# Performance work log

Hardware: AMD Instinct MI355X
Metric: run time of the kernel (lower is better)

## Reference

```python
import jax, jax.numpy as jnp
import numpy as np


def setup_inputs() -> dict:
    key = jax.random.key(0)
    ks = jax.random.split(key, 7)
    B, S, E = 2, 4096, 512
    return {
        "query": jax.random.normal(ks[0], (B, S, E), jnp.float32),
        "key": jax.random.normal(ks[1], (B, S, E), jnp.float32),
        "value": jax.random.normal(ks[2], (B, S, E), jnp.float32),
        "in_proj_weight": jax.random.normal(ks[3], (3 * E, E), jnp.float32) * 0.02,
        "in_proj_bias": jax.random.normal(ks[4], (3 * E,), jnp.float32) * 0.02,
        "out_proj_weight": jax.random.normal(ks[5], (E, E), jnp.float32) * 0.02,
        "out_proj_bias": jax.random.normal(ks[6], (E,), jnp.float32) * 0.02,
        "window_size": 512,
        "stride": 256,
    }


def reference(query, key, value, in_proj_weight, in_proj_bias,
              out_proj_weight, out_proj_bias, window_size, stride):
    B, S, E = query.shape
    H = 8
    hd = E // H
    scale = 1.0 / np.sqrt(hd).astype(np.float32)

    # Project full sequences once (equivalent to projecting each window slice).
    wq, wk, wv = in_proj_weight[:E], in_proj_weight[E:2 * E], in_proj_weight[2 * E:]
    bq, bk, bv = in_proj_bias[:E], in_proj_bias[E:2 * E], in_proj_bias[2 * E:]
    qp = query @ wq.T + bq   # [B,S,E]
    kp = key @ wk.T + bk
    vp = value @ wv.T + bv

    # Overlapping window gather: [nw, W] token indices.
    starts = np.arange(0, S - window_size + 1, stride)
    idx = starts[:, None] + np.arange(window_size)[None, :]  # [nw, W]
    nw, W = idx.shape

    def heads(x):  # [B,S,E] -> [B,nw,W,H,hd]
        return x[:, idx].reshape(B, nw, W, H, hd)

    qh, kh, vh = heads(qp), heads(kp), heads(vp)

    scores = jnp.einsum('bnqhd,bnkhd->bnhqk', qh, kh) * scale  # [B,nw,H,W,W]
    probs = jax.nn.softmax(scores, axis=-1)
    ctx = jnp.einsum('bnhqk,bnkhd->bnqhd', probs, vh)           # [B,nw,W,H,hd]
    ctx = ctx.reshape(B, nw * W, E)                             # concat over windows
    return ctx @ out_proj_weight.T + out_proj_bias              # [B, nw*W, E]
```

## Files before the change

kernel.cpp:

```cpp
#include <hip/hip_runtime.h>
#include <hip/hip_bf16.h>

typedef __bf16 bf16x8 __attribute__((ext_vector_type(8)));
typedef float f32x4 __attribute__((ext_vector_type(4)));
typedef float f32x16 __attribute__((ext_vector_type(16)));

__device__ __forceinline__ ushort f2bf(float f) {
  union { float f; unsigned u; } x; x.f = f;
  unsigned r = x.u + 0x7fffu + ((x.u >> 16) & 1u);
  return (ushort)(r >> 16);
}

__device__ __forceinline__ void gld_lds16(const void* g, void* l) {
  __builtin_amdgcn_global_load_lds(
      (const __attribute__((address_space(1))) void*)g,
      (__attribute__((address_space(3))) void*)l, 16, 0, 0);
}

__global__ __launch_bounds__(256) void k_cvt_w(
    const float* __restrict__ wi, const float* __restrict__ wo,
    ushort* __restrict__ dst) {
  const int NWI = 196608, NWO = 65536;
  const int total = NWI + NWO;
  int i = blockIdx.x * 256 + threadIdx.x;
  int stride = gridDim.x * 256;
  for (; i < total; i += stride) {
    const float* s; int j;
    if (i < NWI) { s = wi; j = i; }
    else         { s = wo; j = i - NWI; }
    float4 val = reinterpret_cast<const float4*>(s)[j];
    ushort4 o;
    o.x = f2bf(val.x); o.y = f2bf(val.y); o.z = f2bf(val.z); o.w = f2bf(val.w);
    reinterpret_cast<ushort4*>(dst)[i] = o;
  }
}

#define GK 512
#define GN 512

__global__ __launch_bounds__(256) void k_gemm_qkv(
    const float* __restrict__ za0, const float* __restrict__ za1,
    const float* __restrict__ za2,
    const ushort* __restrict__ Btbase,
    const float* __restrict__ biasbase,
    ushort* __restrict__ Cbase, float qs)
{
  int z = blockIdx.z;
  const float* A32 = (z == 0) ? za0 : (z == 1) ? za1 : za2;
  const ushort* Bt = Btbase + (size_t)262144 * z;
  const float* bias = biasbase + 512 * z;
  float osc = (z == 0) ? qs : 1.0f;

  __shared__ float  As[128 * 32];
  __shared__ ushort Bs[128 * 32];

  int tid = threadIdx.x;
  int wv = tid >> 6, ln = tid & 63;
  int l15 = ln & 15, lg = ln >> 4;
  int wm = wv >> 1, wn = wv & 1;
  int m0 = blockIdx.x * 128, n0 = blockIdx.y * 128;

  f32x4 acc[4][4] = {};

  for (int kt = 0; kt < 16; ++kt) {
    __syncthreads();
#pragma unroll
    for (int it = 0; it < 4; ++it) {
      int s = it * 256 + tid;
      int row = s >> 3;
      int cs = (s & 7) * 16;
      int gofs = (cs ^ ((row & 7) << 4)) >> 2;
      gld_lds16(A32 + (size_t)(m0 + row) * GK + kt * 32 + gofs,
                (char*)As + (it * 256 + wv * 64) * 16);
    }
#pragma unroll
    for (int h2 = 0; h2 < 2; ++h2) {
      int c = h2 * 256 + wv * 64 + ln;
      int row = c >> 2, kc = (c & 3) * 8;
      gld_lds16(Bt + (size_t)(n0 + row) * GK + kt * 32 + kc,
                (char*)Bs + (h2 * 256 + wv * 64) * 16);
    }
    __syncthreads();

    bf16x8 af[4], bf4[4];
#pragma unroll
    for (int mf = 0; mf < 4; ++mf) {
      int row = wm * 64 + mf * 16 + l15;
      int xr = (row & 7) << 4;
      const char* rb = (const char*)As + row * 128;
      float4 x0 = *reinterpret_cast<const float4*>(rb + ((lg * 32) ^ xr));
      float4 x1 = *reinterpret_cast<const float4*>(rb + (((lg * 32) + 16) ^ xr));
      uint w0, w1, w2, w3;
      asm("v_cvt_pk_bf16_f32 %0, %1, %2" : "=v"(w0) : "v"(x0.x), "v"(x0.y));
      asm("v_cvt_pk_bf16_f32 %0, %1, %2" : "=v"(w1) : "v"(x0.z), "v"(x0.w));
      asm("v_cvt_pk_bf16_f32 %0, %1, %2" : "=v"(w2) : "v"(x1.x), "v"(x1.y));
      asm("v_cvt_pk_bf16_f32 %0, %1, %2" : "=v"(w3) : "v"(x1.z), "v"(x1.w));
      union { uint u[4]; bf16x8 v; } t;
      t.u[0] = w0; t.u[1] = w1; t.u[2] = w2; t.u[3] = w3;
      af[mf] = t.v;
    }
#pragma unroll
    for (int nf = 0; nf < 4; ++nf)
      bf4[nf] = *reinterpret_cast<const bf16x8*>(&Bs[(wn * 64 + nf * 16 + l15) * 32 + lg * 8]);
#pragma unroll
    for (int mf = 0; mf < 4; ++mf)
#pragma unroll
      for (int nf = 0; nf < 4; ++nf)
        acc[mf][nf] = __builtin_amdgcn_mfma_f32_16x16x32_bf16(af[mf], bf4[nf], acc[mf][nf], 0, 0, 0);
  }

#pragma unroll
  for (int mf = 0; mf < 4; ++mf)
#pragma unroll
    for (int nf = 0; nf < 4; ++nf)
#pragma unroll
      for (int r = 0; r < 4; ++r) {
        int rr = m0 + wm * 64 + mf * 16 + lg * 4 + r;
        int cc = n0 + wn * 64 + nf * 16 + l15;
        float v = (acc[mf][nf][r] + bias[cc]) * osc;
        (Cbase + (size_t)4194304 * z)[(size_t)rr * GN + cc] = f2bf(v);
      }
}

__global__ __launch_bounds__(256) void k_gemm_out(
    const ushort* __restrict__ Ab, const ushort* __restrict__ Bt,
    const float* __restrict__ bias, float* __restrict__ C)
{
  __shared__ ushort As[128 * 32];
  __shared__ ushort Bs[128 * 32];

  int tid = threadIdx.x;
  int wv = tid >> 6, ln = tid & 63;
  int l15 = ln & 15, lg = ln >> 4;
  int wm = wv >> 1, wn = wv & 1;
  int m0 = blockIdx.x * 128, n0 = blockIdx.y * 128;

  f32x4 acc[4][4] = {};

  for (int kt = 0; kt < GK / 32; ++kt) {
    __syncthreads();
#pragma unroll
    for (int h2 = 0; h2 < 2; ++h2) {
      int c = h2 * 256 + wv * 64 + ln;
      int row = c >> 2, kc = (c & 3) * 8;
      gld_lds16(Ab + (size_t)(m0 + row) * GK + kt * 32 + kc,
                (char*)As + (h2 * 256 + wv * 64) * 16);
      gld_lds16(Bt + (size_t)(n0 + row) * GK + kt * 32 + kc,
                (char*)Bs + (h2 * 256 + wv * 64) * 16);
    }
    __syncthreads();
    bf16x8 af[4], bf4[4];
#pragma unroll
    for (int mf = 0; mf < 4; ++mf)
      af[mf] = *reinterpret_cast<const bf16x8*>(&As[(wm * 64 + mf * 16 + l15) * 32 + lg * 8]);
#pragma unroll
    for (int nf = 0; nf < 4; ++nf)
      bf4[nf] = *reinterpret_cast<const bf16x8*>(&Bs[(wn * 64 + nf * 16 + l15) * 32 + lg * 8]);
#pragma unroll
    for (int mf = 0; mf < 4; ++mf)
#pragma unroll
      for (int nf = 0; nf < 4; ++nf)
        acc[mf][nf] = __builtin_amdgcn_mfma_f32_16x16x32_bf16(af[mf], bf4[nf], acc[mf][nf], 0, 0, 0);
  }

#pragma unroll
  for (int mf = 0; mf < 4; ++mf)
#pragma unroll
    for (int nf = 0; nf < 4; ++nf)
#pragma unroll
      for (int r = 0; r < 4; ++r) {
        int rr = m0 + wm * 64 + mf * 16 + lg * 4 + r;
        int cc = n0 + wn * 64 + nf * 16 + l15;
        C[(size_t)rr * GN + cc] = acc[mf][nf][r] + bias[cc];
      }
}

__global__ __launch_bounds__(256, 2) void k_attn(
    const ushort* __restrict__ qp, const ushort* __restrict__ kp,
    const ushort* __restrict__ vp, ushort* __restrict__ ctx)
{
  const int E = 512, SEQ = 4096;
  int bid0 = blockIdx.x;
  int bid = (bid0 & 7) * 60 + (bid0 >> 3);
  int qh = bid & 1;
  int h = (bid >> 1) & 7;
  int n = (bid >> 4) % 15;
  int b = bid / 240;
  int start = n * 256;

  int tid = threadIdx.x;
  int w = tid >> 6, ln = tid & 63;
  int l31 = ln & 31, hi = ln >> 5;

  size_t base = ((size_t)(b * SEQ + start)) * E + h * 64;
  const ushort* Kw = kp + base;
  const ushort* Vw = vp + base;
  const ushort* Qw = qp + base;

  __shared__ ushort Vt[32768];

  {
    int sk = (tid & 63) * 8;
    int sd = (tid >> 6) * 16;
    const ushort* src = Vw + (size_t)sk * E + sd;
    union { uint4 q[2]; ushort u[16]; } R0, R1, R2, R3, R4, R5, R6, R7;
    R0.q[0] = *(const uint4*)(src + 0 * E); R0.q[1] = *(const uint4*)(src + 0 * E + 8);
    R1.q[0] = *(const uint4*)(src + 1 * E); R1.q[1] = *(const uint4*)(src + 1 * E + 8);
    R2.q[0] = *(const uint4*)(src + 2 * E); R2.q[1] = *(const uint4*)(src + 2 * E + 8);
    R3.q[0] = *(const uint4*)(src + 3 * E); R3.q[1] = *(const uint4*)(src + 3 * E + 8);
    R4.q[0] = *(const uint4*)(src + 4 * E); R4.q[1] = *(const uint4*)(src + 4 * E + 8);
    R5.q[0] = *(const uint4*)(src + 5 * E); R5.q[1] = *(const uint4*)(src + 5 * E + 8);
    R6.q[0] = *(const uint4*)(src + 6 * E); R6.q[1] = *(const uint4*)(src + 6 * E + 8);
    R7.q[0] = *(const uint4*)(src + 7 * E); R7.q[1] = *(const uint4*)(src + 7 * E + 8);
#pragma unroll
    for (int d0 = 0; d0 < 16; ++d0) {
      int d = sd + d0;
      uint4 val;
      val.x = (uint)R0.u[d0] | ((uint)R1.u[d0] << 16);
      val.y = (uint)R2.u[d0] | ((uint)R3.u[d0] << 16);
      val.z = (uint)R4.u[d0] | ((uint)R5.u[d0] << 16);
      val.w = (uint)R6.u[d0] | ((uint)R7.u[d0] << 16);
      int off = d * 1024 + ((sk * 2) ^ ((d & 7) << 4));
      *(uint4*)((char*)Vt + off) = val;
    }
  }
  __syncthreads();

  int q0 = qh * 256 + w * 64;

  bf16x8 qa0, qa1, qa2, qa3, qb0, qb1, qb2, qb3;
  {
    const ushort* qra = Qw + (size_t)(q0 + l31) * E + hi * 8;
    const ushort* qrb = qra + (size_t)32 * E;
    qa0 = *reinterpret_cast<const bf16x8*>(qra + 0);
    qa1 = *reinterpret_cast<const bf16x8*>(qra + 16);
    qa2 = *reinterpret_cast<const bf16x8*>(qra + 32);
    qa3 = *reinterpret_cast<const bf16x8*>(qra + 48);
    qb0 = *reinterpret_cast<const bf16x8*>(qrb + 0);
    qb1 = *reinterpret_cast<const bf16x8*>(qrb + 16);
    qb2 = *reinterpret_cast<const bf16x8*>(qrb + 32);
    qb3 = *reinterpret_cast<const bf16x8*>(qrb + 48);
  }

  f32x16 ca0 = {}, ca1 = {}, cb0_ = {}, cb1_ = {};
  float psa = 0.f, psb = 0.f;
  const char* lb = (const char*)Vt;

#pragma unroll
  for (int kb = 0; kb < 16; ++kb) {
    bf16x8 kf0, kf1, kf2, kf3;
    {
      const ushort* kr = Kw + (size_t)(kb * 32 + l31) * E + hi * 8;
      kf0 = *reinterpret_cast<const bf16x8*>(kr + 0);
      kf1 = *reinterpret_cast<const bf16x8*>(kr + 16);
      kf2 = *reinterpret_cast<const bf16x8*>(kr + 32);
      kf3 = *reinterpret_cast<const bf16x8*>(kr + 48);
    }
    bf16x8 vb00, vb01, vb10, vb11;
    {
      int row = l31, rowh = 32 + l31;
      int cb0 = kb * 64 + hi * 16;
      int cb1 = cb0 + 32;
      int xr0 = (row & 7) << 4;
      vb00 = *reinterpret_cast<const bf16x8*>(lb + row * 1024 + (cb0 ^ xr0));
      vb01 = *reinterpret_cast<const bf16x8*>(lb + rowh * 1024 + (cb0 ^ xr0));
      vb10 = *reinterpret_cast<const bf16x8*>(lb + row * 1024 + (cb1 ^ xr0));
      vb11 = *reinterpret_cast<const bf16x8*>(lb + rowh * 1024 + (cb1 ^ xr0));
    }

    f32x16 s1 = {}, s2 = {};
    __builtin_amdgcn_s_setprio(1);
    s1 = __builtin_amdgcn_mfma_f32_32x32x16_bf16(kf0, qa0, s1, 0, 0, 0);
    s2 = __builtin_amdgcn_mfma_f32_32x32x16_bf16(kf0, qb0, s2, 0, 0, 0);
    s1 = __builtin_amdgcn_mfma_f32_32x32x16_bf16(kf1, qa1, s1, 0, 0, 0);
    s2 = __builtin_amdgcn_mfma_f32_32x32x16_bf16(kf1, qb1, s2, 0, 0, 0);
    s1 = __builtin_amdgcn_mfma_f32_32x32x16_bf16(kf2, qa2, s1, 0, 0, 0);
    s2 = __builtin_amdgcn_mfma_f32_32x32x16_bf16(kf2, qb2, s2, 0, 0, 0);
    s1 = __builtin_amdgcn_mfma_f32_32x32x16_bf16(kf3, qa3, s1, 0, 0, 0);
    s2 = __builtin_amdgcn_mfma_f32_32x32x16_bf16(kf3, qb3, s2, 0, 0, 0);
    __builtin_amdgcn_s_setprio(0);

#pragma unroll
    for (int r = 0; r < 16; ++r) s1[r] = __builtin_amdgcn_exp2f(s1[r]);
#pragma unroll
    for (int r = 0; r < 16; ++r) s2[r] = __builtin_amdgcn_exp2f(s2[r]);
    {
      float t0 = (s1[0] + s1[1]) + (s1[2] + s1[3]);
      float t1 = (s1[4] + s1[5]) + (s1[6] + s1[7]);
      float t2 = (s1[8] + s1[9]) + (s1[10] + s1[11]);
      float t3 = (s1[12] + s1[13]) + (s1[14] + s1[15]);
      psa += (t0 + t1) + (t2 + t3);
      float u0 = (s2[0] + s2[1]) + (s2[2] + s2[3]);
      float u1 = (s2[4] + s2[5]) + (s2[6] + s2[7]);
      float u2 = (s2[8] + s2[9]) + (s2[10] + s2[11]);
      float u3 = (s2[12] + s2[13]) + (s2[14] + s2[15]);
      psb += (u0 + u1) + (u2 + u3);
    }

    uint a0, a1, a2, a3, a4, a5, a6, a7;
    asm("v_cvt_pk_bf16_f32 %0, %1, %2" : "=v"(a0) : "v"(s1[0]),  "v"(s1[1]));
    asm("v_cvt_pk_bf16_f32 %0, %1, %2" : "=v"(a1) : "v"(s1[2]),  "v"(s1[3]));
    asm("v_cvt_pk_bf16_f32 %0, %1, %2" : "=v"(a2) : "v"(s1[4]),  "v"(s1[5]));
    asm("v_cvt_pk_bf16_f32 %0, %1, %2" : "=v"(a3) : "v"(s1[6]),  "v"(s1[7]));
    asm("v_cvt_pk_bf16_f32 %0, %1, %2" : "=v"(a4) : "v"(s1[8]),  "v"(s1[9]));
    asm("v_cvt_pk_bf16_f32 %0, %1, %2" : "=v"(a5) : "v"(s1[10]), "v"(s1[11]));
    asm("v_cvt_pk_bf16_f32 %0, %1, %2" : "=v"(a6) : "v"(s1[12]), "v"(s1[13]));
    asm("v_cvt_pk_bf16_f32 %0, %1, %2" : "=v"(a7) : "v"(s1[14]), "v"(s1[15]));
    asm("v_permlane32_swap_b32 %0, %1" : "+v"(a0), "+v"(a2));
    asm("v_permlane32_swap_b32 %0, %1" : "+v"(a1), "+v"(a3));
    asm("v_permlane32_swap_b32 %0, %1" : "+v"(a4), "+v"(a6));
    asm("v_permlane32_swap_b32 %0, %1" : "+v"(a5), "+v"(a7));
    uint b0, b1, b2, b3, b4, b5, b6, b7;
    asm("v_cvt_pk_bf16_f32 %0, %1, %2" : "=v"(b0) : "v"(s2[0]),  "v"(s2[1]));
    asm("v_cvt_pk_bf16_f32 %0, %1, %2" : "=v"(b1) : "v"(s2[2]),  "v"(s2[3]));
    asm("v_cvt_pk_bf16_f32 %0, %1, %2" : "=v"(b2) : "v"(s2[4]),  "v"(s2[5]));
    asm("v_cvt_pk_bf16_f32 %0, %1, %2" : "=v"(b3) : "v"(s2[6]),  "v"(s2[7]));
    asm("v_cvt_pk_bf16_f32 %0, %1, %2" : "=v"(b4) : "v"(s2[8]),  "v"(s2[9]));
    asm("v_cvt_pk_bf16_f32 %0, %1, %2" : "=v"(b5) : "v"(s2[10]), "v"(s2[11]));
    asm("v_cvt_pk_bf16_f32 %0, %1, %2" : "=v"(b6) : "v"(s2[12]), "v"(s2[13]));
    asm("v_cvt_pk_bf16_f32 %0, %1, %2" : "=v"(b7) : "v"(s2[14]), "v"(s2[15]));
    asm("v_permlane32_swap_b32 %0, %1" : "+v"(b0), "+v"(b2));
    asm("v_permlane32_swap_b32 %0, %1" : "+v"(b1), "+v"(b3));
    asm("v_permlane32_swap_b32 %0, %1" : "+v"(b4), "+v"(b6));
    asm("v_permlane32_swap_b32 %0, %1" : "+v"(b5), "+v"(b7));
    union { uint u[4]; bf16x8 v; } A1, A2, B1, B2;
    A1.u[0] = a0; A1.u[1] = a1; A1.u[2] = a2; A1.u[3] = a3;
    A2.u[0] = a4; A2.u[1] = a5; A2.u[2] = a6; A2.u[3] = a7;
    B1.u[0] = b0; B1.u[1] = b1; B1.u[2] = b2; B1.u[3] = b3;
    B2.u[0] = b4; B2.u[1] = b5; B2.u[2] = b6; B2.u[3] = b7;

    __builtin_amdgcn_s_setprio(1);
    ca0  = __builtin_amdgcn_mfma_f32_32x32x16_bf16(A1.v, vb00, ca0, 0, 0, 0);
    cb0_ = __builtin_amdgcn_mfma_f32_32x32x16_bf16(B1.v, vb00, cb0_, 0, 0, 0);
    ca1  = __builtin_amdgcn_mfma_f32_32x32x16_bf16(A1.v, vb01, ca1, 0, 0, 0);
    cb1_ = __builtin_amdgcn_mfma_f32_32x32x16_bf16(B1.v, vb01, cb1_, 0, 0, 0);
    ca0  = __builtin_amdgcn_mfma_f32_32x32x16_bf16(A2.v, vb10, ca0, 0, 0, 0);
    cb0_ = __builtin_amdgcn_mfma_f32_32x32x16_bf16(B2.v, vb10, cb0_, 0, 0, 0);
    ca1  = __builtin_amdgcn_mfma_f32_32x32x16_bf16(A2.v, vb11, ca1, 0, 0, 0);
    cb1_ = __builtin_amdgcn_mfma_f32_32x32x16_bf16(B2.v, vb11, cb1_, 0, 0, 0);
    __builtin_amdgcn_s_setprio(0);
  }

  psa += __shfl_xor(psa, 32);
  psb += __shfl_xor(psb, 32);
  float ria = 1.0f / psa;
  float rib = 1.0f / psb;
  size_t orow0 = (size_t)b * 7680 + (size_t)n * 512 + q0;
#pragma unroll
  for (int r = 0; r < 16; ++r) {
    int qrel = (r & 3) + 8 * (r >> 2) + 4 * hi;
    float r1 = __shfl(ria, qrel);
    float r2 = __shfl(rib, qrel);
    ushort* dA = ctx + (orow0 + qrel) * E + h * 64 + l31;
    ushort* dB = ctx + (orow0 + 32 + qrel) * E + h * 64 + l31;
    dA[0]  = f2bf(ca0[r] * r1);
    dA[32] = f2bf(ca1[r] * r1);
    dB[0]  = f2bf(cb0_[r] * r2);
    dB[32] = f2bf(cb1_[r] * r2);
  }
}

extern "C" void kernel_launch(void* const* d_in, const int* in_sizes, int n_in,
                              void* d_out, int out_size, void* d_ws, size_t ws_size,
                              hipStream_t stream) {
  const float* query = (const float*)d_in[0];
  const float* key   = (const float*)d_in[1];
  const float* value = (const float*)d_in[2];
  const float* ipw   = (const float*)d_in[3];
  const float* ipb   = (const float*)d_in[4];
  const float* opw   = (const float*)d_in[5];
  const float* opb   = (const float*)d_in[6];

  ushort* wib = (ushort*)d_ws;
  ushort* wob = wib + 786432;
  ushort* qp  = wob + 262144;
  ushort* kp  = qp  + 4194304;
  ushort* vp  = kp  + 4194304;
  ushort* ctx = vp  + 4194304;

  const float SC = 0.125f * 1.44269504088896340736f;

  k_cvt_w<<<512, 256, 0, stream>>>(ipw, opw, wib);

  k_gemm_qkv<<<dim3(64, 4, 3), 256, 0, stream>>>(
      query, key, value, wib, ipb, qp, SC);

  k_attn<<<480, 256, 0, stream>>>(qp, kp, vp, ctx);

  k_gemm_out<<<dim3(120, 4, 1), 256, 0, stream>>>(
      ctx, wob, opb, (float*)d_out);
}
```

Before: 84.24 us.

## Software-pipeline QKV and output GEMMs with multi-buffered LDS and XCD-aware block swizzle

Result: faster. 81.72 us (-3.0%).

```diff
diff --git a/kernel.cpp b/kernel.cpp
--- a/kernel.cpp
+++ b/kernel.cpp
@@ -16,6 +16,13 @@
       (const __attribute__((address_space(1))) void*)g,
       (__attribute__((address_space(3))) void*)l, 16, 0, 0);
 }
+
+#define VMWAIT2 asm volatile("s_waitcnt vmcnt(2)" ::: "memory")
+#define VMWAIT4 asm volatile("s_waitcnt vmcnt(4)" ::: "memory")
+#define VMWAIT0 asm volatile("s_waitcnt vmcnt(0)" ::: "memory")
+#define LGKM0   asm volatile("s_waitcnt lgkmcnt(0)" ::: "memory")
+#define SCHEDB  __builtin_amdgcn_sched_barrier(0)
+#define RBAR    __builtin_amdgcn_s_barrier()
 
 __global__ __launch_bounds__(256) void k_cvt_w(
     const float* __restrict__ wi, const float* __restrict__ wo,
@@ -35,9 +42,6 @@
   }
 }
 
-#define GK 512
-#define GN 512
-
 __global__ __launch_bounds__(256) void k_gemm_qkv(
     const float* __restrict__ za0, const float* __restrict__ za1,
     const float* __restrict__ za2,
@@ -45,68 +49,106 @@
     const float* __restrict__ biasbase,
     ushort* __restrict__ Cbase, float qs)
 {
-  int z = blockIdx.z;
+  int bid0 = blockIdx.x;
+  int bid = (bid0 & 7) * 96 + (bid0 >> 3);
+  int yy = bid & 3;
+  int rest = bid >> 2;
+  int xx = rest & 63;
+  int z = rest >> 6;
+
   const float* A32 = (z == 0) ? za0 : (z == 1) ? za1 : za2;
   const ushort* Bt = Btbase + (size_t)262144 * z;
   const float* bias = biasbase + 512 * z;
   float osc = (z == 0) ? qs : 1.0f;
 
-  __shared__ float  As[128 * 32];
-  __shared__ ushort Bs[128 * 32];
+  __shared__ ushort As[2][4096];
+  __shared__ ushort Bs[3][4096];
 
   int tid = threadIdx.x;
   int wv = tid >> 6, ln = tid & 63;
   int l15 = ln & 15, lg = ln >> 4;
   int wm = wv >> 1, wn = wv & 1;
-  int m0 = blockIdx.x * 128, n0 = blockIdx.y * 128;
+  int m0 = xx * 128, n0 = yy * 128;
+
+  int row_s = tid >> 1, kh = (tid & 1) * 16;
+  const float* aP = A32 + (size_t)(m0 + row_s) * 512 + kh;
+  int ldsOff = row_s * 32 + kh;
+
+#define STAGE_B(KT, BUF)                                                      \
+  {                                                                           \
+    _Pragma("unroll")                                                         \
+    for (int h2 = 0; h2 < 2; ++h2) {                                          \
+      int c = h2 * 256 + wv * 64 + ln;                                        \
+      int row = c >> 2, kc = (c & 3) * 8;                                     \
+      gld_lds16(Bt + (size_t)(n0 + row) * 512 + (KT) * 32 + kc,               \
+                (char*)&Bs[BUF][0] + (h2 * 256 + wv * 64) * 16);              \
+    }                                                                         \
+  }
+
+#define CVT_WRITE_A(F0, F1, F2, F3, BUF)                                      \
+  {                                                                           \
+    uint w0, w1, w2, w3, w4, w5, w6, w7;                                      \
+    asm("v_cvt_pk_bf16_f32 %0, %1, %2" : "=v"(w0) : "v"(F0.x), "v"(F0.y));    \
+    asm("v_cvt_pk_bf16_f32 %0, %1, %2" : "=v"(w1) : "v"(F0.z), "v"(F0.w));    \
+    asm("v_cvt_pk_bf16_f32 %0, %1, %2" : "=v"(w2) : "v"(F1.x), "v"(F1.y));    \
+    asm("v_cvt_pk_bf16_f32 %0, %1, %2" : "=v"(w3) : "v"(F1.z), "v"(F1.w));    \
+    asm("v_cvt_pk_bf16_f32 %0, %1, %2" : "=v"(w4) : "v"(F2.x), "v"(F2.y));    \
+    asm("v_cvt_pk_bf16_f32 %0, %1, %2" : "=v"(w5) : "v"(F2.z), "v"(F2.w));    \
+    asm("v_cvt_pk_bf16_f32 %0, %1, %2" : "=v"(w6) : "v"(F3.x), "v"(F3.y));    \
+    asm("v_cvt_pk_bf16_f32 %0, %1, %2" : "=v"(w7) : "v"(F3.z), "v"(F3.w));    \
+    uint4 p0; p0.x = w0; p0.y = w1; p0.z = w2; p0.w = w3;                     \
+    uint4 p1; p1.x = w4; p1.y = w5; p1.z = w6; p1.w = w7;                     \
+    reinterpret_cast<uint4*>(&As[BUF][ldsOff])[0] = p0;                       \
+    reinterpret_cast<uint4*>(&As[BUF][ldsOff + 8])[0] = p1;                   \
+  }
 
   f32x4 acc[4][4] = {};
 
+  STAGE_B(0, 0);
+  float4 g0 = reinterpret_cast<const float4*>(aP)[0];
+  float4 g1 = reinterpret_cast<const float4*>(aP)[1];
+  float4 g2 = reinterpret_cast<const float4*>(aP)[2];
+  float4 g3 = reinterpret_cast<const float4*>(aP)[3];
+  STAGE_B(1, 1);
+  VMWAIT2; SCHEDB;
+  CVT_WRITE_A(g0, g1, g2, g3, 0);
+  LGKM0; SCHEDB;
+  RBAR;
+
+#pragma unroll
   for (int kt = 0; kt < 16; ++kt) {
-    __syncthreads();
-#pragma unroll
-    for (int it = 0; it < 4; ++it) {
-      int s = it * 256 + tid;
-      int row = s >> 3;
-      int cs = (s & 7) * 16;
-      int gofs = (cs ^ ((row & 7) << 4)) >> 2;
-      gld_lds16(A32 + (size_t)(m0 + row) * GK + kt * 32 + gofs,
-                (char*)As + (it * 256 + wv * 64) * 16);
-    }
-#pragma unroll
-    for (int h2 = 0; h2 < 2; ++h2) {
-      int c = h2 * 256 + wv * 64 + ln;
-      int row = c >> 2, kc = (c & 3) * 8;
-      gld_lds16(Bt + (size_t)(n0 + row) * GK + kt * 32 + kc,
-                (char*)Bs + (h2 * 256 + wv * 64) * 16);
-    }
-    __syncthreads();
+    const int cur = kt & 1;
+    const int bcur = kt % 3;
+    float4 f0, f1, f2, f3;
+    if (kt < 15) {
+      const float* ap = aP + (kt + 1) * 32;
+      f0 = reinterpret_cast<const float4*>(ap)[0];
+      f1 = reinterpret_cast<const float4*>(ap)[1];
+      f2 = reinterpret_cast<const float4*>(ap)[2];
+      f3 = reinterpret_cast<const float4*>(ap)[3];
+    }
+    if (kt < 14) STAGE_B(kt + 2, (kt + 2) % 3);
 
     bf16x8 af[4], bf4[4];
 #pragma unroll
-    for (int mf = 0; mf < 4; ++mf) {
-      int row = wm * 64 + mf * 16 + l15;
-      int xr = (row & 7) << 4;
-      const char* rb = (const char*)As + row * 128;
-      float4 x0 = *reinterpret_cast<const float4*>(rb + ((lg * 32) ^ xr));
-      float4 x1 = *reinterpret_cast<const float4*>(rb + (((lg * 32) + 16) ^ xr));
-      uint w0, w1, w2, w3;
-      asm("v_cvt_pk_bf16_f32 %0, %1, %2" : "=v"(w0) : "v"(x0.x), "v"(x0.y));
-      asm("v_cvt_pk_bf16_f32 %0, %1, %2" : "=v"(w1) : "v"(x0.z), "v"(x0.w));
-      asm("v_cvt_pk_bf16_f32 %0, %1, %2" : "=v"(w2) : "v"(x1.x), "v"(x1.y));
-      asm("v_cvt_pk_bf16_f32 %0, %1, %2" : "=v"(w3) : "v"(x1.z), "v"(x1.w));
-      union { uint u[4]; bf16x8 v; } t;
-      t.u[0] = w0; t.u[1] = w1; t.u[2] = w2; t.u[3] = w3;
-      af[mf] = t.v;
-    }
+    for (int mf = 0; mf < 4; ++mf)
+      af[mf] = *reinterpret_cast<const bf16x8*>(&As[cur][(wm * 64 + mf * 16 + l15) * 32 + lg * 8]);
 #pragma unroll
     for (int nf = 0; nf < 4; ++nf)
-      bf4[nf] = *reinterpret_cast<const bf16x8*>(&Bs[(wn * 64 + nf * 16 + l15) * 32 + lg * 8]);
+      bf4[nf] = *reinterpret_cast<const bf16x8*>(&Bs[bcur][(wn * 64 + nf * 16 + l15) * 32 + lg * 8]);
 #pragma unroll
     for (int mf = 0; mf < 4; ++mf)
 #pragma unroll
       for (int nf = 0; nf < 4; ++nf)
         acc[mf][nf] = __builtin_amdgcn_mfma_f32_16x16x32_bf16(af[mf], bf4[nf], acc[mf][nf], 0, 0, 0);
+
+    if (kt < 15) {
+      if (kt < 14) { VMWAIT2; } else { VMWAIT0; }
+      SCHEDB;
+      CVT_WRITE_A(f0, f1, f2, f3, cur ^ 1);
+      LGKM0; SCHEDB;
+      RBAR;
+    }
   }
 
 #pragma unroll
@@ -118,49 +160,73 @@
         int rr = m0 + wm * 64 + mf * 16 + lg * 4 + r;
         int cc = n0 + wn * 64 + nf * 16 + l15;
         float v = (acc[mf][nf][r] + bias[cc]) * osc;
-        (Cbase + (size_t)4194304 * z)[(size_t)rr * GN + cc] = f2bf(v);
+        (Cbase + (size_t)4194304 * z)[(size_t)rr * 512 + cc] = f2bf(v);
       }
+#undef STAGE_B
+#undef CVT_WRITE_A
 }
 
 __global__ __launch_bounds__(256) void k_gemm_out(
     const ushort* __restrict__ Ab, const ushort* __restrict__ Bt,
     const float* __restrict__ bias, float* __restrict__ C)
 {
-  __shared__ ushort As[128 * 32];
-  __shared__ ushort Bs[128 * 32];
+  int bid0 = blockIdx.x;
+  int bid = (bid0 & 7) * 60 + (bid0 >> 3);
+  int yy = bid & 3;
+  int xx = bid >> 2;
+
+  __shared__ ushort As[3][4096];
+  __shared__ ushort Bs[3][4096];
 
   int tid = threadIdx.x;
   int wv = tid >> 6, ln = tid & 63;
   int l15 = ln & 15, lg = ln >> 4;
   int wm = wv >> 1, wn = wv & 1;
-  int m0 = blockIdx.x * 128, n0 = blockIdx.y * 128;
+  int m0 = xx * 128, n0 = yy * 128;
+
+#define STAGE_AB(KT, BUF)                                                     \
+  {                                                                           \
+    _Pragma("unroll")                                                         \
+    for (int h2 = 0; h2 < 2; ++h2) {                                          \
+      int c = h2 * 256 + wv * 64 + ln;                                        \
+      int row = c >> 2, kc = (c & 3) * 8;                                     \
+      gld_lds16(Ab + (size_t)(m0 + row) * 512 + (KT) * 32 + kc,               \
+                (char*)&As[BUF][0] + (h2 * 256 + wv * 64) * 16);              \
+      gld_lds16(Bt + (size_t)(n0 + row) * 512 + (KT) * 32 + kc,               \
+                (char*)&Bs[BUF][0] + (h2 * 256 + wv * 64) * 16);              \
+    }                                                                         \
+  }
 
   f32x4 acc[4][4] = {};
 
-  for (int kt = 0; kt < GK / 32; ++kt) {
-    __syncthreads();
-#pragma unroll
-    for (int h2 = 0; h2 < 2; ++h2) {
-      int c = h2 * 256 + wv * 64 + ln;
-      int row = c >> 2, kc = (c & 3) * 8;
-      gld_lds16(Ab + (size_t)(m0 + row) * GK + kt * 32 + kc,
-                (char*)As + (h2 * 256 + wv * 64) * 16);
-      gld_lds16(Bt + (size_t)(n0 + row) * GK + kt * 32 + kc,
-                (char*)Bs + (h2 * 256 + wv * 64) * 16);
-    }
-    __syncthreads();
+  STAGE_AB(0, 0);
+  STAGE_AB(1, 1);
+  VMWAIT4; SCHEDB;
+  RBAR;
+
+#pragma unroll
+  for (int kt = 0; kt < 16; ++kt) {
+    const int bcur = kt % 3;
+    if (kt < 14) STAGE_AB(kt + 2, (kt + 2) % 3);
+
     bf16x8 af[4], bf4[4];
 #pragma unroll
     for (int mf = 0; mf < 4; ++mf)
-      af[mf] = *reinterpret_cast<const bf16x8*>(&As[(wm * 64 + mf * 16 + l15) * 32 + lg * 8]);
+      af[mf] = *reinterpret_cast<const bf16x8*>(&As[bcur][(wm * 64 + mf * 16 + l15) * 32 + lg * 8]);
 #pragma unroll
     for (int nf = 0; nf < 4; ++nf)
-      bf4[nf] = *reinterpret_cast<const bf16x8*>(&Bs[(wn * 64 + nf * 16 + l15) * 32 + lg * 8]);
+      bf4[nf] = *reinterpret_cast<const bf16x8*>(&Bs[bcur][(wn * 64 + nf * 16 + l15) * 32 + lg * 8]);
 #pragma unroll
     for (int mf = 0; mf < 4; ++mf)
 #pragma unroll
       for (int nf = 0; nf < 4; ++nf)
         acc[mf][nf] = __builtin_amdgcn_mfma_f32_16x16x32_bf16(af[mf], bf4[nf], acc[mf][nf], 0, 0, 0);
+
+    if (kt < 15) {
+      if (kt < 14) { VMWAIT4; } else { VMWAIT0; }
+      SCHEDB;
+      RBAR;
+    }
   }
 
 #pragma unroll
@@ -171,8 +237,9 @@
       for (int r = 0; r < 4; ++r) {
         int rr = m0 + wm * 64 + mf * 16 + lg * 4 + r;
         int cc = n0 + wn * 64 + nf * 16 + l15;
-        C[(size_t)rr * GN + cc] = acc[mf][nf][r] + bias[cc];
+        C[(size_t)rr * 512 + cc] = acc[mf][nf][r] + bias[cc];
       }
+#undef STAGE_AB
 }
 
 __global__ __launch_bounds__(256, 2) void k_attn(
@@ -382,11 +449,11 @@
 
   k_cvt_w<<<512, 256, 0, stream>>>(ipw, opw, wib);
 
-  k_gemm_qkv<<<dim3(64, 4, 3), 256, 0, stream>>>(
+  k_gemm_qkv<<<768, 256, 0, stream>>>(
       query, key, value, wib, ipb, qp, SC);
 
   k_attn<<<480, 256, 0, stream>>>(qp, kp, vp, ctx);
 
-  k_gemm_out<<<dim3(120, 4, 1), 256, 0, stream>>>(
+  k_gemm_out<<<480, 256, 0, stream>>>(
       ctx, wob, opb, (float*)d_out);
 }
```
